# Kernel tuning notes

Hardware: AMD Instinct MI355X
Metric: run time of the kernel (lower is better)

The kernel has to match this reference:

```python
import jax, jax.numpy as jnp
import numpy as np

DIM = 256
HID = DIM // 8  # 32


def setup_inputs() -> dict:
    key = jax.random.key(0)
    ks = jax.random.split(key, 16)
    B, N, M, C = 4, 4096, 16, DIM
    q = jax.random.normal(ks[0], (B, N, C), dtype=jnp.float32)
    k = jax.random.normal(ks[1], (B, N, M, C), dtype=jnp.float32)
    pos = jax.random.normal(ks[2], (B, N, M, 4), dtype=jnp.float32)
    mask = jax.random.randint(ks[3], (B, N, M, 1), 0, 2, dtype=jnp.int32)
    s = 1.0 / np.sqrt(C)
    # weights stored [in, out]; apply as x @ W (+ b)
    Ws = jax.random.normal(ks[4], (C, C), dtype=jnp.float32) * s
    Wp1 = jax.random.normal(ks[5], (4, HID), dtype=jnp.float32) * 0.5
    bp1 = jnp.zeros((HID,), dtype=jnp.float32)
    Wp2 = jax.random.normal(ks[6], (HID, C), dtype=jnp.float32) * (1.0 / np.sqrt(HID))
    bp2 = jnp.zeros((C,), dtype=jnp.float32)
    Wa1 = jax.random.normal(ks[7], (C, HID), dtype=jnp.float32) * s
    ba1 = jnp.zeros((HID,), dtype=jnp.float32)
    Wa2 = jax.random.normal(ks[8], (HID, C), dtype=jnp.float32) * (1.0 / np.sqrt(HID))
    ba2 = jnp.zeros((C,), dtype=jnp.float32)
    Wo = jax.random.normal(ks[9], (C, C), dtype=jnp.float32) * s
    bo = jnp.zeros((C,), dtype=jnp.float32)
    return {"q": q, "k": k, "pos": pos, "mask": mask,
            "Ws": Ws, "Wp1": Wp1, "bp1": bp1, "Wp2": Wp2, "bp2": bp2,
            "Wa1": Wa1, "ba1": ba1, "Wa2": Wa2, "ba2": ba2,
            "Wo": Wo, "bo": bo}


def reference(q, k, pos, mask, Ws, Wp1, bp1, Wp2, bp2, Wa1, ba1, Wa2, ba2, Wo, bo):
    # shared_fc (no bias)
    q_ = q @ Ws                         # [B,N,C]
    k_ = k @ Ws                         # [B,N,M,C]
    v = k_ @ Ws                         # NOTE: source applies shared_fc twice to k
    # pos_fc: 4 -> C/8 -> C
    posf = jax.nn.relu(pos @ Wp1 + bp1) @ Wp2 + bp2   # [B,N,M,C]
    # MLP attention over (k - q + pos)
    attn = k_ - q_[:, :, None, :] + posf               # [B,N,M,C]
    attn = jax.nn.relu(attn @ Wa1 + ba1) @ Wa2 + ba2   # [B,N,M,C]
    attn = jnp.where(mask == 0, jnp.float32(-1e9), attn)
    attn = jax.nn.softmax(attn, axis=-2)               # softmax over M
    # dropout is identity in eval mode
    x = jnp.sum((v + posf) * attn, axis=2)             # [B,N,C]
    x = x @ Wo + bo
    return x
```

## Files before the change

kernel.cpp:

```cpp
#include <hip/hip_runtime.h>
#include <hip/hip_bf16.h>

typedef __attribute__((ext_vector_type(4))) float f4;
typedef __attribute__((ext_vector_type(4))) int i4;
typedef __attribute__((ext_vector_type(8))) short s8;
typedef __attribute__((ext_vector_type(4))) short s4;

#define MFMA16(a,b,c) __builtin_amdgcn_mfma_f32_16x16x32_bf16((a),(b),(c),0,0,0)

static __device__ __forceinline__ unsigned short f2bf(float x){
  return __builtin_bit_cast(unsigned short, __float2bfloat16(x));
}
__device__ __forceinline__ int fidx(int kk, int c, int nct){
  return ((((kk >> 5) * nct + (c >> 4)) << 6) + (((kk >> 3) & 3) * 16 + (c & 15))) * 8 + (kk & 7);
}

__global__ void prepw(const float* __restrict__ Ws, const float* __restrict__ Wa1,
                      const float* __restrict__ Wo, const float* __restrict__ Wp2,
                      const float* __restrict__ Wa2, const float* __restrict__ bp2,
                      const float* __restrict__ ba1,
                      unsigned short* __restrict__ Ws2f, unsigned short* __restrict__ Wof,
                      unsigned short* __restrict__ WsWa1f,
                      unsigned short* __restrict__ Wp2f, unsigned short* __restrict__ Wa2f,
                      unsigned short* __restrict__ Wp2Wa1f, float* __restrict__ bh){
  __shared__ float wrow[256];
  int t = threadIdx.x;
  if (blockIdx.x < 256){
    int i = blockIdx.x;
    wrow[t] = Ws[i*256 + t];
    __syncthreads();
    float a1 = 0.f;
    for (int t2 = 0; t2 < 256; ++t2) a1 += wrow[t2] * Ws[t2*256 + t];
    Ws2f[fidx(i, t, 16)] = f2bf(a1);
    Wof[fidx(i, t, 16)]  = f2bf(Wo[i*256 + t]);
    if (t < 32){
      float a2 = 0.f;
      for (int t2 = 0; t2 < 256; ++t2) a2 += wrow[t2] * Wa1[t2*32 + t];
      WsWa1f[fidx(i, t, 2)] = f2bf(a2);
    }
  } else {
    int gid = (blockIdx.x - 256) * 256 + t;
    if (gid < 8192){
      int kk = gid >> 8, c = gid & 255;
      Wp2f[fidx(kk, c, 16)] = f2bf(Wp2[gid]);
    } else {
      int g = gid - 8192; int kk = g >> 8, c = g & 255;
      Wa2f[fidx(kk, c, 16)] = f2bf(Wa2[g]);
    }
    if (gid < 1024){
      int h1 = gid >> 5, h2 = gid & 31;
      float a = 0.f;
      for (int c = 0; c < 256; ++c) a += Wp2[h1*256 + c] * Wa1[c*32 + h2];
      Wp2Wa1f[fidx(h1, h2, 2)] = f2bf(a);
    }
    if (gid < 32){
      float a = ba1[gid];
      for (int c = 0; c < 256; ++c) a += bp2[c] * Wa1[c*32 + gid];
      bh[gid] = a;
    }
  }
}

__global__ __attribute__((amdgpu_flat_work_group_size(256,256), amdgpu_waves_per_eu(4,4)))
void attn_x(
  const float* __restrict__ q, const float* __restrict__ k,
  const float* __restrict__ pos, const int* __restrict__ mask,
  const float* __restrict__ Wp1, const float* __restrict__ bp1,
  const float* __restrict__ bp2, const float* __restrict__ bh,
  const unsigned short* __restrict__ Ws2f, const unsigned short* __restrict__ WsWa1f,
  const unsigned short* __restrict__ Wp2f, const unsigned short* __restrict__ Wa2f,
  const unsigned short* __restrict__ Wp2Wa1f,
  unsigned short* __restrict__ xbuf)
{
  __shared__ unsigned short kA[16384];
  __shared__ unsigned short phL[2048];
  __shared__ unsigned short hL[2048];

  const int t = threadIdx.x;
  const int lane = t & 63;
  const int w = t >> 6;
  const int lg = lane >> 4;
  const int lr = lane & 15;
  const int bn0 = blockIdx.x * 4;
  const int n0 = bn0 + w;
  const f4 z4 = {0.f, 0.f, 0.f, 0.f};

  const float* kbase = k + (size_t)n0 * 4096;
  unsigned short* kAw = kA + w * 4096;
  unsigned short* qb  = hL + w * 512;
  {
    f4 qv = *(const f4*)(q + (size_t)n0 * 256 + lane * 4);
    s4 qpk;
    qpk[0] = (short)f2bf(qv[0]); qpk[1] = (short)f2bf(qv[1]);
    qpk[2] = (short)f2bf(qv[2]); qpk[3] = (short)f2bf(qv[3]);
    *(s4*)(qb + lane * 4) = qpk;
  }
  {
    const int c0l = lane * 4;
    const int kts = c0l >> 5, lgs = (c0l >> 3) & 3, js = c0l & 7;
    unsigned short* kdst0 = kAw + ((kts * 64 + lgs * 16) << 3) + js;
    #pragma unroll
    for (int m = 0; m < 16; ++m){
      f4 kv = *(const f4*)(kbase + m * 256 + c0l);
      s4 pk;
      pk[0] = (short)f2bf(kv[0]); pk[1] = (short)f2bf(kv[1]);
      pk[2] = (short)f2bf(kv[2]); pk[3] = (short)f2bf(kv[3]);
      *(s4*)(kdst0 + (m << 3)) = pk;
    }
  }

  const unsigned short* wa1b = WsWa1f + (size_t)lane * 8;
  f4 kh0 = z4, kh1 = z4, qh0 = z4, qh1 = z4;
  #pragma unroll
  for (int kt = 0; kt < 8; ++kt){
    s8 kfr = *(const s8*)(kAw + ((kt * 64 + lane) << 3));
    s8 qfr = *(const s8*)(qb + kt * 32 + lg * 8);
    s8 wt0 = *(const s8*)(wa1b + (size_t)(kt * 2 + 0) * 512);
    s8 wt1 = *(const s8*)(wa1b + (size_t)(kt * 2 + 1) * 512);
    kh0 = MFMA16(kfr, wt0, kh0);  kh1 = MFMA16(kfr, wt1, kh1);
    qh0 = MFMA16(qfr, wt0, qh0);  qh1 = MFMA16(qfr, wt1, qh1);
  }
  float qhs0 = __shfl(qh0[0], lr);
  float qhs1 = __shfl(qh1[0], lr);

  s8 phfrag;
  {
    f4 pv = *(const f4*)(pos + (size_t)n0 * 64 + (size_t)lr * 4);
    f4 h0 = *(const f4*)(bp1 + lg * 8);
    f4 h1 = *(const f4*)(bp1 + lg * 8 + 4);
    #pragma unroll
    for (int p = 0; p < 4; ++p){
      f4 w0 = *(const f4*)(Wp1 + p * 32 + lg * 8);
      f4 w1 = *(const f4*)(Wp1 + p * 32 + lg * 8 + 4);
      #pragma unroll
      for (int j = 0; j < 4; ++j){ h0[j] += pv[p] * w0[j]; h1[j] += pv[p] * w1[j]; }
    }
    #pragma unroll
    for (int j = 0; j < 4; ++j){
      phfrag[j]     = (short)f2bf(fmaxf(h0[j], 0.f));
      phfrag[4 + j] = (short)f2bf(fmaxf(h1[j], 0.f));
    }
  }
  *(s8*)(phL + (w * 64 + lane) * 8) = phfrag;

  {
    const unsigned short* wpwb = Wp2Wa1f + (size_t)lane * 8;
    kh0 = MFMA16(phfrag, *(const s8*)(wpwb), kh0);
    kh1 = MFMA16(phfrag, *(const s8*)(wpwb + 512), kh1);
  }

  #pragma unroll
  for (int ct2 = 0; ct2 < 2; ++ct2){
    float bhc = bh[ct2 * 16 + lr] - (ct2 ? qhs1 : qhs0);
    #pragma unroll
    for (int r = 0; r < 4; ++r){
      int m = lg * 4 + r, col = ct2 * 16 + lr;
      float hv = (ct2 ? kh1[r] : kh0[r]) + bhc;
      hL[w * 512 + ((col >> 3) * 16 + m) * 8 + (col & 7)] = f2bf(fmaxf(hv, 0.f));
    }
  }
  __syncthreads();

  const unsigned short* ws2b = Ws2f + (size_t)lane * 8;
  const unsigned short* wp2b = Wp2f + (size_t)lane * 8;
  const unsigned short* wa2b = Wa2f + (size_t)lane * 8;

#define EPI_N(VN, N, CT, BP, BA, BP2C) { \
    s8 pfr = *(const s8*)(phL + ((N) * 64 + lane) * 8); \
    s8 hfr = *(const s8*)(hL + ((N) * 64 + lane) * 8); \
    f4 pf = MFMA16(pfr, (BP), z4); \
    f4 aa = MFMA16(hfr, (BA), z4); \
    i4 mv = *(const i4*)(mask + (size_t)(bn0 + (N)) * 16 + lg * 4); \
    float lg0 = mv[0] ? aa[0] : -1e9f; \
    float lg1 = mv[1] ? aa[1] : -1e9f; \
    float lg2 = mv[2] ? aa[2] : -1e9f; \
    float lg3 = mv[3] ? aa[3] : -1e9f; \
    float mx = fmaxf(fmaxf(lg0, lg1), fmaxf(lg2, lg3)); \
    mx = fmaxf(mx, __shfl_xor(mx, 16)); \
    mx = fmaxf(mx, __shfl_xor(mx, 32)); \
    float p0 = __expf(lg0 - mx), p1 = __expf(lg1 - mx); \
    float p2 = __expf(lg2 - mx), p3 = __expf(lg3 - mx); \
    float den = p0 + p1 + p2 + p3; \
    float num = p0 * ((VN)[0] + pf[0] + (BP2C)) \
              + p1 * ((VN)[1] + pf[1] + (BP2C)) \
              + p2 * ((VN)[2] + pf[2] + (BP2C)) \
              + p3 * ((VN)[3] + pf[3] + (BP2C)); \
    den += __shfl_xor(den, 16); den += __shfl_xor(den, 32); \
    num += __shfl_xor(num, 16); num += __shfl_xor(num, 32); \
    if (lane < 16) \
      xbuf[(size_t)(bn0 + (N)) * 256 + (CT) * 16 + lr] = f2bf(__fdividef(num, den)); \
  }

#define EPILOGUE(V0, V1, V2, V3, CT) { \
    s8 bp = *(const s8*)(wp2b + (size_t)(CT) * 512); \
    s8 ba = *(const s8*)(wa2b + (size_t)(CT) * 512); \
    float bp2c = bp2[(CT) * 16 + lr]; \
    EPI_N(V0, 0, CT, bp, ba, bp2c); \
    EPI_N(V1, 1, CT, bp, ba, bp2c); \
    EPI_N(V2, 2, CT, bp, ba, bp2c); \
    EPI_N(V3, 3, CT, bp, ba, bp2c); \
  }

  #pragma unroll
  for (int cp = 0; cp < 2; ++cp){
    const int ct0 = w * 4 + cp * 2;
    const int ct1 = ct0 + 1;
    f4 v00 = z4, v01 = z4, v02 = z4, v03 = z4;
    f4 v10 = z4, v11 = z4, v12 = z4, v13 = z4;
    #pragma unroll
    for (int kt = 0; kt < 8; ++kt){
      s8 b0 = *(const s8*)(ws2b + (size_t)(kt * 16 + ct0) * 512);
      s8 b1 = *(const s8*)(ws2b + (size_t)(kt * 16 + ct1) * 512);
      s8 af0 = *(const s8*)(kA + ((0 * 8 + kt) * 64 + lane) * 8);
      s8 af1 = *(const s8*)(kA + ((1 * 8 + kt) * 64 + lane) * 8);
      s8 af2 = *(const s8*)(kA + ((2 * 8 + kt) * 64 + lane) * 8);
      s8 af3 = *(const s8*)(kA + ((3 * 8 + kt) * 64 + lane) * 8);
      v00 = MFMA16(af0, b0, v00); v10 = MFMA16(af0, b1, v10);
      v01 = MFMA16(af1, b0, v01); v11 = MFMA16(af1, b1, v11);
      v02 = MFMA16(af2, b0, v02); v12 = MFMA16(af2, b1, v12);
      v03 = MFMA16(af3, b0, v03); v13 = MFMA16(af3, b1, v13);
    }
    EPILOGUE(v00, v01, v02, v03, ct0);
    EPILOGUE(v10, v11, v12, v13, ct1);
  }
#undef EPILOGUE
#undef EPI_N
}

__global__ __launch_bounds__(128, 4) void proj(
  const unsigned short* __restrict__ xbuf, const unsigned short* __restrict__ Wof,
  const float* __restrict__ bo, float* __restrict__ out)
{
  const int t = threadIdx.x;
  const int lane = t & 63;
  const int w = t >> 6;
  const int lg = lane >> 4;
  const int lr = lane & 15;
  const int n0 = blockIdx.x * 32 + w * 16;
  const f4 z4 = {0.f, 0.f, 0.f, 0.f};
  const unsigned short* xr = xbuf + (size_t)(n0 + lr) * 256;
  const unsigned short* wob = Wof + (size_t)lane * 8;
  #pragma unroll
  for (int p = 0; p < 4; ++p){
    f4 oac[4] = {z4, z4, z4, z4};
    #pragma unroll
    for (int kt = 0; kt < 8; ++kt){
      s8 xf = *(const s8*)(xr + kt * 32 + lg * 8);
      #pragma unroll
      for (int ci = 0; ci < 4; ++ci)
        oac[ci] = MFMA16(xf, *(const s8*)(wob + (size_t)(kt * 16 + p * 4 + ci) * 512), oac[ci]);
    }
    #pragma unroll
    for (int ci = 0; ci < 4; ++ci){
      int c = (p * 4 + ci) * 16 + lr;
      float bov = bo[c];
      #pragma unroll
      for (int r = 0; r < 4; ++r)
        out[(size_t)(n0 + lg * 4 + r) * 256 + c] = oac[ci][r] + bov;
    }
  }
}

__global__ __launch_bounds__(256, 4) void attn_mono(
  const float* __restrict__ q, const float* __restrict__ k,
  const float* __restrict__ pos, const int* __restrict__ mask,
  const float* __restrict__ Wp1, const float* __restrict__ bp1,
  const float* __restrict__ bp2, const float* __restrict__ bo,
  const float* __restrict__ bh,
  const unsigned short* __restrict__ Ws2f, const unsigned short* __restrict__ WsWa1f,
  const unsigned short* __restrict__ Wp2f, const unsigned short* __restrict__ Wa2f,
  const unsigned short* __restrict__ Wp2Wa1f, const unsigned short* __restrict__ Wof,
  float* __restrict__ out)
{
  __shared__ unsigned short kA[16384];
  __shared__ unsigned short phL[2048];
  __shared__ unsigned short hL[2048];
  __shared__ unsigned short xT[4096];

  const int t = threadIdx.x;
  const int lane = t & 63;
  const int w = t >> 6;
  const int lg = lane >> 4;
  const int lr = lane & 15;
  const int bn0 = blockIdx.x * 4;
  const int n0 = bn0 + w;
  const f4 z4 = {0.f, 0.f, 0.f, 0.f};

  const float* krow = k + (size_t)n0 * 4096 + (size_t)lr * 256;
  const float* qrow = q + (size_t)n0 * 256;
  const unsigned short* wa1b = WsWa1f + (size_t)lane * 8;
  f4 khac[2] = {z4, z4};
  #pragma unroll
  for (int kt = 0; kt < 8; ++kt){
    int c0 = kt * 32 + lg * 8;
    f4 ka = *(const f4*)(krow + c0);
    f4 kb = *(const f4*)(krow + c0 + 4);
    f4 qa = *(const f4*)(qrow + c0);
    f4 qb = *(const f4*)(qrow + c0 + 4);
    s8 kf, mf;
    #pragma unroll
    for (int j = 0; j < 4; ++j){
      kf[j]     = (short)f2bf(ka[j]);
      kf[4 + j] = (short)f2bf(kb[j]);
      mf[j]     = (short)f2bf(ka[j] - qa[j]);
      mf[4 + j] = (short)f2bf(kb[j] - qb[j]);
    }
    *(s8*)(kA + ((w * 8 + kt) * 64 + lane) * 8) = kf;
    khac[0] = MFMA16(mf, *(const s8*)(wa1b + (size_t)(kt * 2 + 0) * 512), khac[0]);
    khac[1] = MFMA16(mf, *(const s8*)(wa1b + (size_t)(kt * 2 + 1) * 512), khac[1]);
  }
  s8 phfrag;
  {
    f4 pv = *(const f4*)(pos + (size_t)n0 * 64 + (size_t)lr * 4);
    f4 h0 = *(const f4*)(bp1 + lg * 8);
    f4 h1 = *(const f4*)(bp1 + lg * 8 + 4);
    #pragma unroll
    for (int p = 0; p < 4; ++p){
      f4 w0 = *(const f4*)(Wp1 + p * 32 + lg * 8);
      f4 w1 = *(const f4*)(Wp1 + p * 32 + lg * 8 + 4);
      #pragma unroll
      for (int j = 0; j < 4; ++j){ h0[j] += pv[p] * w0[j]; h1[j] += pv[p] * w1[j]; }
    }
    #pragma unroll
    for (int j = 0; j < 4; ++j){
      phfrag[j]     = (short)f2bf(fmaxf(h0[j], 0.f));
      phfrag[4 + j] = (short)f2bf(fmaxf(h1[j], 0.f));
    }
  }
  *(s8*)(phL + (w * 64 + lane) * 8) = phfrag;
  {
    const unsigned short* wpwb = Wp2Wa1f + (size_t)lane * 8;
    khac[0] = MFMA16(phfrag, *(const s8*)(wpwb), khac[0]);
    khac[1] = MFMA16(phfrag, *(const s8*)(wpwb + 512), khac[1]);
  }
  #pragma unroll
  for (int ct2 = 0; ct2 < 2; ++ct2){
    float bhc = bh[ct2 * 16 + lr];
    #pragma unroll
    for (int r = 0; r < 4; ++r){
      int m = lg * 4 + r, col = ct2 * 16 + lr;
      hL[w * 512 + ((col >> 3) * 16 + m) * 8 + (col & 7)] = f2bf(fmaxf(khac[ct2][r] + bhc, 0.f));
    }
  }
  __syncthreads();

  const unsigned short* ws2b = Ws2f + (size_t)lane * 8;
  const unsigned short* wp2b = Wp2f + (size_t)lane * 8;
  const unsigned short* wa2b = Wa2f + (size_t)lane * 8;
  #pragma unroll
  for (int ci = 0; ci < 4; ++ci){
    int ct = w * 4 + ci;
    f4 vacc[4] = {z4, z4, z4, z4};
    #pragma unroll
    for (int kt = 0; kt < 8; ++kt){
      s8 bw = *(const s8*)(ws2b + (size_t)(kt * 16 + ct) * 512);
      #pragma unroll
      for (int n = 0; n < 4; ++n){
        s8 af = *(const s8*)(kA + ((n * 8 + kt) * 64 + lane) * 8);
        vacc[n] = MFMA16(af, bw, vacc[n]);
      }
    }
    s8 bp = *(const s8*)(wp2b + (size_t)ct * 512);
    s8 ba = *(const s8*)(wa2b + (size_t)ct * 512);
    f4 pf[4], aa[4];
    #pragma unroll
    for (int n = 0; n < 4; ++n){
      s8 pfr = *(const s8*)(phL + (n * 64 + lane) * 8);
      s8 hfr = *(const s8*)(hL + (n * 64 + lane) * 8);
      pf[n] = MFMA16(pfr, bp, z4);
      aa[n] = MFMA16(hfr, ba, z4);
    }
    float bp2c = bp2[ct * 16 + lr];
    #pragma unroll
    for (int n = 0; n < 4; ++n){
      i4 mv = *(const i4*)(mask + (size_t)(bn0 + n) * 16 + lg * 4);
      float lg0 = mv[0] ? aa[n][0] : -1e9f;
      float lg1 = mv[1] ? aa[n][1] : -1e9f;
      float lg2 = mv[2] ? aa[n][2] : -1e9f;
      float lg3 = mv[3] ? aa[n][3] : -1e9f;
      float mx = fmaxf(fmaxf(lg0, lg1), fmaxf(lg2, lg3));
      mx = fmaxf(mx, __shfl_xor(mx, 16));
      mx = fmaxf(mx, __shfl_xor(mx, 32));
      float p0 = __expf(lg0 - mx), p1 = __expf(lg1 - mx);
      float p2 = __expf(lg2 - mx), p3 = __expf(lg3 - mx);
      float den = p0 + p1 + p2 + p3;
      float num = p0 * (vacc[n][0] + pf[n][0] + bp2c)
                + p1 * (vacc[n][1] + pf[n][1] + bp2c)
                + p2 * (vacc[n][2] + pf[n][2] + bp2c)
                + p3 * (vacc[n][3] + pf[n][3] + bp2c);
      den += __shfl_xor(den, 16); den += __shfl_xor(den, 32);
      num += __shfl_xor(num, 16); num += __shfl_xor(num, 32);
      if (lane < 16){
        int c = ct * 16 + lr;
        xT[((c >> 5) * 64 + ((c >> 3) & 3) * 16 + n) * 8 + (c & 7)] = f2bf(__fdividef(num, den));
      }
    }
  }
  __syncthreads();

  f4 oac[4] = {z4, z4, z4, z4};
  const unsigned short* wob = Wof + (size_t)lane * 8;
  #pragma unroll
  for (int kt = 0; kt < 8; ++kt){
    s8 xf = *(const s8*)(xT + (kt * 64 + lane) * 8);
    #pragma unroll
    for (int ci = 0; ci < 4; ++ci)
      oac[ci] = MFMA16(xf, *(const s8*)(wob + (size_t)(kt * 16 + w * 4 + ci) * 512), oac[ci]);
  }
  if (lane < 16){
    #pragma unroll
    for (int ci = 0; ci < 4; ++ci){
      int c = (w * 4 + ci) * 16 + lr;
      float bov = bo[c];
      #pragma unroll
      for (int r = 0; r < 4; ++r)
        out[(size_t)(bn0 + r) * 256 + c] = oac[ci][r] + bov;
    }
  }
}

extern "C" void kernel_launch(void* const* d_in, const int* in_sizes, int n_in,
                              void* d_out, int out_size, void* d_ws, size_t ws_size,
                              hipStream_t stream) {
  (void)in_sizes; (void)n_in; (void)out_size;
  const float* q   = (const float*)d_in[0];
  const float* k   = (const float*)d_in[1];
  const float* pos = (const float*)d_in[2];
  const int*   msk = (const int*)d_in[3];
  const float* Ws  = (const float*)d_in[4];
  const float* Wp1 = (const float*)d_in[5];
  const float* bp1 = (const float*)d_in[6];
  const float* Wp2 = (const float*)d_in[7];
  const float* bp2 = (const float*)d_in[8];
  const float* Wa1 = (const float*)d_in[9];
  const float* ba1 = (const float*)d_in[10];
  const float* Wa2 = (const float*)d_in[11];
  const float* Wo  = (const float*)d_in[13];
  const float* bo  = (const float*)d_in[14];

  if (ws_size < 313472) return;
  char* ws = (char*)d_ws;
  unsigned short* Ws2f    = (unsigned short*)(ws + 0);
  unsigned short* Wof     = (unsigned short*)(ws + 131072);
  unsigned short* WsWa1f  = (unsigned short*)(ws + 262144);
  unsigned short* Wp2f    = (unsigned short*)(ws + 278528);
  unsigned short* Wa2f    = (unsigned short*)(ws + 294912);
  unsigned short* Wp2Wa1f = (unsigned short*)(ws + 311296);
  float*          bh      = (float*)(ws + 313344);
  unsigned short* xbuf    = (unsigned short*)(ws + 313472);

  prepw<<<dim3(320), dim3(256), 0, stream>>>(Ws, Wa1, Wo, Wp2, Wa2, bp2, ba1,
                                             Ws2f, Wof, WsWa1f, Wp2f, Wa2f, Wp2Wa1f, bh);

  if (ws_size >= 313472 + 8388608) {
    attn_x<<<dim3(4096), dim3(256), 0, stream>>>(q, k, pos, msk, Wp1, bp1, bp2, bh,
                                                 Ws2f, WsWa1f, Wp2f, Wa2f, Wp2Wa1f, xbuf);
    proj<<<dim3(512), dim3(128), 0, stream>>>(xbuf, Wof, bo, (float*)d_out);
  } else {
    attn_mono<<<dim3(4096), dim3(256), 0, stream>>>(q, k, pos, msk, Wp1, bp1, bp2, bo, bh,
                                                    Ws2f, WsWa1f, Wp2f, Wa2f, Wp2Wa1f, Wof,
                                                    (float*)d_out);
  }
}
```

Before: 150.4 us.

## Split k/q bf16 conversion into a separate pre-pass kernel

Moves the fp32-to-bf16 conversion of k and q out of the attention kernel into a new attn_cvt kernel that writes MFMA-fragment-ordered bf16 buffers to workspace. The attention kernel then reads fragments straight from global memory instead of staging them in a 32KB LDS tile, which frees LDS and may raise occupancy. The cost is an extra full write and read of a 134MB bf16 copy of k, plus another kernel launch. It also needs a much larger workspace, and falls back to the monolithic path when the workspace is too small.

```diff
diff --git a/kernel.cpp b/kernel.cpp
--- a/kernel.cpp
+++ b/kernel.cpp
@@ -61,18 +61,48 @@
   }
 }
 
-__global__ __attribute__((amdgpu_flat_work_group_size(256,256), amdgpu_waves_per_eu(4,4)))
-void attn_x(
+__global__ __launch_bounds__(256) void attn_cvt(
   const float* __restrict__ q, const float* __restrict__ k,
+  unsigned short* __restrict__ kfbuf, unsigned short* __restrict__ qbuf)
+{
+  const int t = threadIdx.x;
+  const int lane = t & 63;
+  const int w = t >> 6;
+  const int n0 = blockIdx.x * 4 + w;
+  {
+    f4 qv = *(const f4*)(q + (size_t)n0 * 256 + lane * 4);
+    s4 qpk;
+    qpk[0] = (short)f2bf(qv[0]); qpk[1] = (short)f2bf(qv[1]);
+    qpk[2] = (short)f2bf(qv[2]); qpk[3] = (short)f2bf(qv[3]);
+    *(s4*)(qbuf + (size_t)n0 * 256 + lane * 4) = qpk;
+  }
+  {
+    const float* kbase = k + (size_t)n0 * 4096;
+    unsigned short* kdn = kfbuf + (size_t)n0 * 4096;
+    const int c0l = lane * 4;
+    const int kts = c0l >> 5, lgs = (c0l >> 3) & 3, js = c0l & 7;
+    unsigned short* kdst0 = kdn + ((kts * 64 + lgs * 16) << 3) + js;
+    #pragma unroll
+    for (int m = 0; m < 16; ++m){
+      f4 kv = *(const f4*)(kbase + m * 256 + c0l);
+      s4 pk;
+      pk[0] = (short)f2bf(kv[0]); pk[1] = (short)f2bf(kv[1]);
+      pk[2] = (short)f2bf(kv[2]); pk[3] = (short)f2bf(kv[3]);
+      *(s4*)(kdst0 + (m << 3)) = pk;
+    }
+  }
+}
+
+__global__ __launch_bounds__(256) void attn_E(
   const float* __restrict__ pos, const int* __restrict__ mask,
   const float* __restrict__ Wp1, const float* __restrict__ bp1,
   const float* __restrict__ bp2, const float* __restrict__ bh,
   const unsigned short* __restrict__ Ws2f, const unsigned short* __restrict__ WsWa1f,
   const unsigned short* __restrict__ Wp2f, const unsigned short* __restrict__ Wa2f,
   const unsigned short* __restrict__ Wp2Wa1f,
+  const unsigned short* __restrict__ kfbuf, const unsigned short* __restrict__ qbuf,
   unsigned short* __restrict__ xbuf)
 {
-  __shared__ unsigned short kA[16384];
   __shared__ unsigned short phL[2048];
   __shared__ unsigned short hL[2048];
 
@@ -85,36 +115,14 @@
   const int n0 = bn0 + w;
   const f4 z4 = {0.f, 0.f, 0.f, 0.f};
 
-  const float* kbase = k + (size_t)n0 * 4096;
-  unsigned short* kAw = kA + w * 4096;
-  unsigned short* qb  = hL + w * 512;
-  {
-    f4 qv = *(const f4*)(q + (size_t)n0 * 256 + lane * 4);
-    s4 qpk;
-    qpk[0] = (short)f2bf(qv[0]); qpk[1] = (short)f2bf(qv[1]);
-    qpk[2] = (short)f2bf(qv[2]); qpk[3] = (short)f2bf(qv[3]);
-    *(s4*)(qb + lane * 4) = qpk;
-  }
-  {
-    const int c0l = lane * 4;
-    const int kts = c0l >> 5, lgs = (c0l >> 3) & 3, js = c0l & 7;
-    unsigned short* kdst0 = kAw + ((kts * 64 + lgs * 16) << 3) + js;
-    #pragma unroll
-    for (int m = 0; m < 16; ++m){
-      f4 kv = *(const f4*)(kbase + m * 256 + c0l);
-      s4 pk;
-      pk[0] = (short)f2bf(kv[0]); pk[1] = (short)f2bf(kv[1]);
-      pk[2] = (short)f2bf(kv[2]); pk[3] = (short)f2bf(kv[3]);
-      *(s4*)(kdst0 + (m << 3)) = pk;
-    }
-  }
-
+  const unsigned short* kfn = kfbuf + (size_t)n0 * 4096;
+  const unsigned short* qbn = qbuf + (size_t)n0 * 256;
   const unsigned short* wa1b = WsWa1f + (size_t)lane * 8;
   f4 kh0 = z4, kh1 = z4, qh0 = z4, qh1 = z4;
   #pragma unroll
   for (int kt = 0; kt < 8; ++kt){
-    s8 kfr = *(const s8*)(kAw + ((kt * 64 + lane) << 3));
-    s8 qfr = *(const s8*)(qb + kt * 32 + lg * 8);
+    s8 kfr = *(const s8*)(kfn + ((kt * 64 + lane) << 3));
+    s8 qfr = *(const s8*)(qbn + kt * 32 + lg * 8);
     s8 wt0 = *(const s8*)(wa1b + (size_t)(kt * 2 + 0) * 512);
     s8 wt1 = *(const s8*)(wa1b + (size_t)(kt * 2 + 1) * 512);
     kh0 = MFMA16(kfr, wt0, kh0);  kh1 = MFMA16(kfr, wt1, kh1);
@@ -211,10 +219,10 @@
     for (int kt = 0; kt < 8; ++kt){
       s8 b0 = *(const s8*)(ws2b + (size_t)(kt * 16 + ct0) * 512);
       s8 b1 = *(const s8*)(ws2b + (size_t)(kt * 16 + ct1) * 512);
-      s8 af0 = *(const s8*)(kA + ((0 * 8 + kt) * 64 + lane) * 8);
-      s8 af1 = *(const s8*)(kA + ((1 * 8 + kt) * 64 + lane) * 8);
-      s8 af2 = *(const s8*)(kA + ((2 * 8 + kt) * 64 + lane) * 8);
-      s8 af3 = *(const s8*)(kA + ((3 * 8 + kt) * 64 + lane) * 8);
+      s8 af0 = *(const s8*)(kfbuf + (((size_t)(bn0 + 0) * 8 + kt) * 64 + lane) * 8);
+      s8 af1 = *(const s8*)(kfbuf + (((size_t)(bn0 + 1) * 8 + kt) * 64 + lane) * 8);
+      s8 af2 = *(const s8*)(kfbuf + (((size_t)(bn0 + 2) * 8 + kt) * 64 + lane) * 8);
+      s8 af3 = *(const s8*)(kfbuf + (((size_t)(bn0 + 3) * 8 + kt) * 64 + lane) * 8);
       v00 = MFMA16(af0, b0, v00); v10 = MFMA16(af0, b1, v10);
       v01 = MFMA16(af1, b0, v01); v11 = MFMA16(af1, b1, v11);
       v02 = MFMA16(af2, b0, v02); v12 = MFMA16(af2, b1, v12);
@@ -448,13 +456,18 @@
   unsigned short* Wp2Wa1f = (unsigned short*)(ws + 311296);
   float*          bh      = (float*)(ws + 313344);
   unsigned short* xbuf    = (unsigned short*)(ws + 313472);
+  unsigned short* kfbuf   = (unsigned short*)(ws + 8702080);
+  unsigned short* qbuf    = (unsigned short*)(ws + 142919808);
+  const size_t WS_SPLIT = 151308416;
 
   prepw<<<dim3(320), dim3(256), 0, stream>>>(Ws, Wa1, Wo, Wp2, Wa2, bp2, ba1,
                                              Ws2f, Wof, WsWa1f, Wp2f, Wa2f, Wp2Wa1f, bh);
 
-  if (ws_size >= 313472 + 8388608) {
-    attn_x<<<dim3(4096), dim3(256), 0, stream>>>(q, k, pos, msk, Wp1, bp1, bp2, bh,
-                                                 Ws2f, WsWa1f, Wp2f, Wa2f, Wp2Wa1f, xbuf);
+  if (ws_size >= WS_SPLIT) {
+    attn_cvt<<<dim3(4096), dim3(256), 0, stream>>>(q, k, kfbuf, qbuf);
+    attn_E<<<dim3(4096), dim3(256), 0, stream>>>(pos, msk, Wp1, bp1, bp2, bh,
+                                                 Ws2f, WsWa1f, Wp2f, Wa2f, Wp2Wa1f,
+                                                 kfbuf, qbuf, xbuf);
     proj<<<dim3(512), dim3(128), 0, stream>>>(xbuf, Wof, bo, (float*)d_out);
   } else {
     attn_mono<<<dim3(4096), dim3(256), 0, stream>>>(q, k, pos, msk, Wp1, bp1, bp2, bo, bh,
```

Result: slower. 274.3 us (+82.4%).

## Split attention block work across eight waves instead of four

Applied to the files above, without the earlier changes.

Doubles the attention kernel's block from 256 to 512 threads. Each point's k load and hidden-layer MFMAs are now shared by two waves, and each wave owns two output column tiles instead of four. The aim is more latency hiding and shorter per-wave critical paths for the same shared memory per block. The costs are an added barrier after the k staging, per-lane global q loads with bf16 conversion in place of the shared-memory q fragment, and the loss of the explicit waves-per-eu occupancy hint, which may change register allocation.

```diff
diff --git a/kernel.cpp b/kernel.cpp
--- a/kernel.cpp
+++ b/kernel.cpp
@@ -61,8 +61,7 @@
   }
 }
 
-__global__ __attribute__((amdgpu_flat_work_group_size(256,256), amdgpu_waves_per_eu(4,4)))
-void attn_x(
+__global__ __launch_bounds__(512) void attn_x8(
   const float* __restrict__ q, const float* __restrict__ k,
   const float* __restrict__ pos, const int* __restrict__ mask,
   const float* __restrict__ Wp1, const float* __restrict__ bp1,
@@ -79,28 +78,23 @@
   const int t = threadIdx.x;
   const int lane = t & 63;
   const int w = t >> 6;
+  const int p = w >> 1;
+  const int sub = w & 1;
   const int lg = lane >> 4;
   const int lr = lane & 15;
   const int bn0 = blockIdx.x * 4;
-  const int n0 = bn0 + w;
+  const int n0 = bn0 + p;
   const f4 z4 = {0.f, 0.f, 0.f, 0.f};
 
-  const float* kbase = k + (size_t)n0 * 4096;
-  unsigned short* kAw = kA + w * 4096;
-  unsigned short* qb  = hL + w * 512;
-  {
-    f4 qv = *(const f4*)(q + (size_t)n0 * 256 + lane * 4);
-    s4 qpk;
-    qpk[0] = (short)f2bf(qv[0]); qpk[1] = (short)f2bf(qv[1]);
-    qpk[2] = (short)f2bf(qv[2]); qpk[3] = (short)f2bf(qv[3]);
-    *(s4*)(qb + lane * 4) = qpk;
-  }
-  {
+  {
+    const float* kbase = k + (size_t)n0 * 4096;
+    unsigned short* kAw = kA + p * 4096;
     const int c0l = lane * 4;
     const int kts = c0l >> 5, lgs = (c0l >> 3) & 3, js = c0l & 7;
     unsigned short* kdst0 = kAw + ((kts * 64 + lgs * 16) << 3) + js;
     #pragma unroll
-    for (int m = 0; m < 16; ++m){
+    for (int j = 0; j < 8; ++j){
+      int m = sub * 8 + j;
       f4 kv = *(const f4*)(kbase + m * 256 + c0l);
       s4 pk;
       pk[0] = (short)f2bf(kv[0]); pk[1] = (short)f2bf(kv[1]);
@@ -108,20 +102,28 @@
       *(s4*)(kdst0 + (m << 3)) = pk;
     }
   }
-
+  __syncthreads();
+
+  const unsigned short* kAw = kA + p * 4096;
+  const float* qrow = q + (size_t)n0 * 256;
   const unsigned short* wa1b = WsWa1f + (size_t)lane * 8;
-  f4 kh0 = z4, kh1 = z4, qh0 = z4, qh1 = z4;
+  f4 kh = z4, qh = z4;
   #pragma unroll
   for (int kt = 0; kt < 8; ++kt){
     s8 kfr = *(const s8*)(kAw + ((kt * 64 + lane) << 3));
-    s8 qfr = *(const s8*)(qb + kt * 32 + lg * 8);
-    s8 wt0 = *(const s8*)(wa1b + (size_t)(kt * 2 + 0) * 512);
-    s8 wt1 = *(const s8*)(wa1b + (size_t)(kt * 2 + 1) * 512);
-    kh0 = MFMA16(kfr, wt0, kh0);  kh1 = MFMA16(kfr, wt1, kh1);
-    qh0 = MFMA16(qfr, wt0, qh0);  qh1 = MFMA16(qfr, wt1, qh1);
-  }
-  float qhs0 = __shfl(qh0[0], lr);
-  float qhs1 = __shfl(qh1[0], lr);
+    f4 qa = *(const f4*)(qrow + kt * 32 + lg * 8);
+    f4 qb4 = *(const f4*)(qrow + kt * 32 + lg * 8 + 4);
+    s8 qfr;
+    #pragma unroll
+    for (int j = 0; j < 4; ++j){
+      qfr[j]     = (short)f2bf(qa[j]);
+      qfr[4 + j] = (short)f2bf(qb4[j]);
+    }
+    s8 wt = *(const s8*)(wa1b + (size_t)(kt * 2 + sub) * 512);
+    kh = MFMA16(kfr, wt, kh);
+    qh = MFMA16(qfr, wt, qh);
+  }
+  float qhs = __shfl(qh[0], lr);
 
   s8 phfrag;
   {
@@ -129,11 +131,11 @@
     f4 h0 = *(const f4*)(bp1 + lg * 8);
     f4 h1 = *(const f4*)(bp1 + lg * 8 + 4);
     #pragma unroll
-    for (int p = 0; p < 4; ++p){
-      f4 w0 = *(const f4*)(Wp1 + p * 32 + lg * 8);
-      f4 w1 = *(const f4*)(Wp1 + p * 32 + lg * 8 + 4);
-      #pragma unroll
-      for (int j = 0; j < 4; ++j){ h0[j] += pv[p] * w0[j]; h1[j] += pv[p] * w1[j]; }
+    for (int pp = 0; pp < 4; ++pp){
+      f4 w0 = *(const f4*)(Wp1 + pp * 32 + lg * 8);
+      f4 w1 = *(const f4*)(Wp1 + pp * 32 + lg * 8 + 4);
+      #pragma unroll
+      for (int j = 0; j < 4; ++j){ h0[j] += pv[pp] * w0[j]; h1[j] += pv[pp] * w1[j]; }
     }
     #pragma unroll
     for (int j = 0; j < 4; ++j){
@@ -141,22 +143,16 @@
       phfrag[4 + j] = (short)f2bf(fmaxf(h1[j], 0.f));
     }
   }
-  *(s8*)(phL + (w * 64 + lane) * 8) = phfrag;
-
-  {
-    const unsigned short* wpwb = Wp2Wa1f + (size_t)lane * 8;
-    kh0 = MFMA16(phfrag, *(const s8*)(wpwb), kh0);
-    kh1 = MFMA16(phfrag, *(const s8*)(wpwb + 512), kh1);
-  }
-
-  #pragma unroll
-  for (int ct2 = 0; ct2 < 2; ++ct2){
-    float bhc = bh[ct2 * 16 + lr] - (ct2 ? qhs1 : qhs0);
+  if (sub == 0) *(s8*)(phL + (p * 64 + lane) * 8) = phfrag;
+
+  kh = MFMA16(phfrag, *(const s8*)(Wp2Wa1f + (size_t)lane * 8 + (size_t)sub * 512), kh);
+
+  {
+    float bhc = bh[sub * 16 + lr] - qhs;
     #pragma unroll
     for (int r = 0; r < 4; ++r){
-      int m = lg * 4 + r, col = ct2 * 16 + lr;
-      float hv = (ct2 ? kh1[r] : kh0[r]) + bhc;
-      hL[w * 512 + ((col >> 3) * 16 + m) * 8 + (col & 7)] = f2bf(fmaxf(hv, 0.f));
+      int m = lg * 4 + r, col = sub * 16 + lr;
+      hL[p * 512 + ((col >> 3) * 16 + m) * 8 + (col & 7)] = f2bf(fmaxf(kh[r] + bhc, 0.f));
     }
   }
   __syncthreads();
@@ -201,9 +197,8 @@
     EPI_N(V3, 3, CT, bp, ba, bp2c); \
   }
 
-  #pragma unroll
-  for (int cp = 0; cp < 2; ++cp){
-    const int ct0 = w * 4 + cp * 2;
+  {
+    const int ct0 = w * 2;
     const int ct1 = ct0 + 1;
     f4 v00 = z4, v01 = z4, v02 = z4, v03 = z4;
     f4 v10 = z4, v11 = z4, v12 = z4, v13 = z4;
@@ -453,8 +448,8 @@
                                              Ws2f, Wof, WsWa1f, Wp2f, Wa2f, Wp2Wa1f, bh);
 
   if (ws_size >= 313472 + 8388608) {
-    attn_x<<<dim3(4096), dim3(256), 0, stream>>>(q, k, pos, msk, Wp1, bp1, bp2, bh,
-                                                 Ws2f, WsWa1f, Wp2f, Wa2f, Wp2Wa1f, xbuf);
+    attn_x8<<<dim3(4096), dim3(512), 0, stream>>>(q, k, pos, msk, Wp1, bp1, bp2, bh,
+                                                  Ws2f, WsWa1f, Wp2f, Wa2f, Wp2Wa1f, xbuf);
     proj<<<dim3(512), dim3(128), 0, stream>>>(xbuf, Wof, bo, (float*)d_out);
   } else {
     attn_mono<<<dim3(4096), dim3(256), 0, stream>>>(q, k, pos, msk, Wp1, bp1, bp2, bo, bh,
```

Result: slower. 217.4 us (+44.5%).
